# Kernel optimization log

Hardware: AMD Instinct MI355X
Metric: run time of the kernel (lower is better)

## Reference

```python
import jax, jax.numpy as jnp
import numpy as np

B, S, W = 128, 48, 12          # batch, sentences, words per sentence (= max_seq)
V, SYM, H = 32000, 128, 256    # vocab, symbol_size, hidden_size
E, R = 48, 24                  # entity_size, role_size
EPS = 1e-6


def _mlp(x, W1, b1, W2, b2):
    # repo MLP: tanh on both layers
    h = jnp.tanh(jnp.einsum('...e,eh->...h', x, W1) + b1)
    return jnp.tanh(jnp.einsum('...h,ho->...o', h, W2) + b2)


def _layer_norm(x, gain, bias):
    mu = x.mean(-1, keepdims=True)
    var = ((x - mu) ** 2).mean(-1, keepdims=True)
    return gain * (x - mu) / jnp.sqrt(var + EPS) + bias


def setup_inputs() -> dict:
    key = jax.random.key(0)
    ks = jax.random.split(key, 16)
    p = lambda k, shp: (jax.random.normal(k, shp) * 0.05).astype(jnp.float32)
    return {
        'story': jax.random.randint(ks[0], (B, S, W), 0, V),
        'query': jax.random.randint(ks[1], (B, W), 0, V),
        'word_embed': jax.random.uniform(ks[2], (V, SYM), minval=-0.1, maxval=0.1, dtype=jnp.float32),
        'pos_embed': jnp.ones((W, SYM), jnp.float32) / W,
        'Z': p(ks[3], (E, V)),
        # update-module MLPs: 2 entity heads, 3 role heads (stacked on dim 0)
        'ue_W1': p(ks[4], (2, SYM, H)), 'ue_b1': jnp.zeros((2, H), jnp.float32),
        'ue_W2': p(ks[5], (2, H, E)),   'ue_b2': jnp.zeros((2, E), jnp.float32),
        'ur_W1': p(ks[6], (3, SYM, H)), 'ur_b1': jnp.zeros((3, H), jnp.float32),
        'ur_W2': p(ks[7], (3, H, R)),   'ur_b2': jnp.zeros((3, R), jnp.float32),
        # inference-module MLPs
        'ie_W1': p(ks[8], (2, SYM, H)), 'ie_b1': jnp.zeros((2, H), jnp.float32),
        'ie_W2': p(ks[9], (2, H, E)),   'ie_b2': jnp.zeros((2, E), jnp.float32),
        'ir_W1': p(ks[10], (3, SYM, H)), 'ir_b1': jnp.zeros((3, H), jnp.float32),
        'ir_W2': p(ks[11], (3, H, R)),   'ir_b2': jnp.zeros((3, R), jnp.float32),
        # 3 optional LayerNorms over entity dim
        'ln_gain': jnp.ones((3, E), jnp.float32),
        'ln_bias': jnp.zeros((3, E), jnp.float32),
    }


def reference(story, query, word_embed, pos_embed, Z,
              ue_W1, ue_b1, ue_W2, ue_b2, ur_W1, ur_b1, ur_W2, ur_b2,
              ie_W1, ie_b1, ie_W2, ie_b2, ir_W1, ir_b1, ir_W2, ir_b2,
              ln_gain, ln_bias):
    # ---- UpdateModule ----
    sent = word_embed[story]                                   # [B,S,W,SYM]
    ssum = jnp.einsum('bswe,we->bse', sent, pos_embed)         # [B,S,SYM]
    e1 = _mlp(ssum, ue_W1[0], ue_b1[0], ue_W2[0], ue_b2[0])    # [B,S,E]
    e2 = _mlp(ssum, ue_W1[1], ue_b1[1], ue_W2[1], ue_b2[1])
    r1 = _mlp(ssum, ur_W1[0], ur_b1[0], ur_W2[0], ur_b2[0])    # [B,S,R]
    r2 = _mlp(ssum, ur_W1[1], ur_b1[1], ur_W2[1], ur_b2[1])
    r3 = _mlp(ssum, ur_W1[2], ur_b1[2], ur_W2[2], ur_b2[2])
    paW = jnp.einsum('bsr,bsf->bsrf', r1, e2)                  # partial_add_W
    paB = jnp.einsum('bsr,bsf->bsrf', r3, e1)                  # partial_add_B

    def step(TPR, x):
        e1i, e2i, r1i, r2i, r3i, paWi, paBi = x
        w_hat = jnp.einsum('be,br,berf->bf', e1i, r1i, TPR)
        m_hat = jnp.einsum('be,br,berf->bf', e1i, r2i, TPR)
        b_hat = jnp.einsum('be,br,berf->bf', e2i, r3i, TPR)
        write_op = paWi - jnp.einsum('br,bf->brf', r1i, w_hat)
        move_op = jnp.einsum('br,bf->brf', r2i, w_hat) - jnp.einsum('br,bf->brf', r2i, m_hat)
        backlink_op = paBi - jnp.einsum('br,bf->brf', r3i, b_hat)
        delta = (jnp.einsum('be,brf->berf', e1i, write_op + move_op)
                 + jnp.einsum('be,brf->berf', e2i, backlink_op))
        return TPR + delta, None

    xs = tuple(jnp.swapaxes(t, 0, 1) for t in (e1, e2, r1, r2, r3, paW, paB))  # step-major
    TPR0 = jnp.zeros((story.shape[0], E, R, E), jnp.float32)
    TPR, _ = jax.lax.scan(step, TPR0, xs)

    # ---- InferenceModule ----
    qsum = jnp.einsum('bwe,we->be', word_embed[query], pos_embed)  # [B,SYM]
    qe1 = _mlp(qsum, ie_W1[0], ie_b1[0], ie_W2[0], ie_b2[0])
    qr1 = _mlp(qsum, ir_W1[0], ir_b1[0], ir_W2[0], ir_b2[0])
    qr2 = _mlp(qsum, ir_W1[1], ir_b1[1], ir_W2[1], ir_b2[1])
    qr3 = _mlp(qsum, ir_W1[2], ir_b1[2], ir_W2[2], ir_b2[2])
    i1 = _layer_norm(jnp.einsum('be,br,berf->bf', qe1, qr1, TPR), ln_gain[0], ln_bias[0])
    i2 = _layer_norm(jnp.einsum('be,br,berf->bf', i1, qr2, TPR), ln_gain[1], ln_bias[1])
    i3 = _layer_norm(jnp.einsum('be,br,berf->bf', i2, qr3, TPR), ln_gain[2], ln_bias[2])
    logits = jnp.einsum('bf,fl->bl', i1 + i2 + i3, Z)              # [B,V]
    return logits
```

## Files before the change

### kernel.cpp

```cpp
#include <hip/hip_runtime.h>
#include <hip/hip_bf16.h>

#define B_ 128
#define S_ 48
#define W_ 12
#define V_ 32000
#define SYM_ 128
#define H_ 256
#define E_ 48
#define R_ 24
#define TM 32

typedef float f32x4 __attribute__((ext_vector_type(4)));

__device__ __forceinline__ float4 fma4(float s, float4 w, float4 a) {
    a.x = fmaf(s, w.x, a.x); a.y = fmaf(s, w.y, a.y);
    a.z = fmaf(s, w.z, a.z); a.w = fmaf(s, w.w, a.w);
    return a;
}

__device__ __forceinline__ void gl_lds16(const float* g, float* l) {
    __builtin_amdgcn_global_load_lds(
        (const __attribute__((address_space(1))) void*)g,
        (__attribute__((address_space(3))) void*)l, 16, 0, 0);
}

__device__ __forceinline__ float dot48(const float* A, const float* Bp) {
    const float4* a = reinterpret_cast<const float4*>(A);
    const float4* b4 = reinterpret_cast<const float4*>(Bp);
    float4 acc = {0.f, 0.f, 0.f, 0.f};
#pragma unroll
    for (int i = 0; i < 12; ++i) {
        float4 x = a[i], y = b4[i];
        acc.x = fmaf(x.x, y.x, acc.x); acc.y = fmaf(x.y, y.y, acc.y);
        acc.z = fmaf(x.z, y.z, acc.z); acc.w = fmaf(x.w, y.w, acc.w);
    }
    return (acc.x + acc.y) + (acc.z + acc.w);
}
__device__ __forceinline__ float dot24(const float* A, const float* Bp) {
    const float4* a = reinterpret_cast<const float4*>(A);
    const float4* b4 = reinterpret_cast<const float4*>(Bp);
    float4 acc = {0.f, 0.f, 0.f, 0.f};
#pragma unroll
    for (int i = 0; i < 6; ++i) {
        float4 x = a[i], y = b4[i];
        acc.x = fmaf(x.x, y.x, acc.x); acc.y = fmaf(x.y, y.y, acc.y);
        acc.z = fmaf(x.z, y.z, acc.z); acc.w = fmaf(x.w, y.w, acc.w);
    }
    return (acc.x + acc.y) + (acc.z + acc.w);
}

__global__ __launch_bounds__(128) void ssum_kernel(
    const int* __restrict__ story, const int* __restrict__ query,
    const float* __restrict__ we, const float* __restrict__ pe,
    float* __restrict__ ssum, float* __restrict__ qsum)
{
    int i = blockIdx.x;
    int c = threadIdx.x;
    const int* idxp;
    float* outp;
    if (i < B_ * S_) {
        idxp = story + (size_t)i * W_;
        outp = ssum + (size_t)i * SYM_;
    } else {
        int b = i - B_ * S_;
        idxp = query + (size_t)b * W_;
        outp = qsum + (size_t)b * SYM_;
    }
    float acc = 0.f;
#pragma unroll
    for (int w = 0; w < W_; ++w) {
        int id = idxp[w];
        acc = fmaf(we[(size_t)id * SYM_ + c], pe[w * SYM_ + c], acc);
    }
    outp[c] = acc;
}

template<int NQ>
__device__ __forceinline__ void mlp_layer2(
    int t, int row0, const float4* hs4, const float* __restrict__ W2,
    const float* __restrict__ b2, float* __restrict__ out)
{
    const float4* W2_4 = reinterpret_cast<const float4*>(W2);
    for (int idx = t; idx < TM * NQ; idx += 256) {
        int row = idx / NQ, q = idx - row * NQ;
        float4 cw0 = W2_4[0 * NQ + q];
        float4 cw1 = W2_4[1 * NQ + q];
        float4 cw2 = W2_4[2 * NQ + q];
        float4 cw3 = W2_4[3 * NQ + q];
        float4 a = {0, 0, 0, 0};
#pragma unroll 1
        for (int k4 = 0; k4 < H_ / 4 - 1; ++k4) {
            float4 nw0 = W2_4[(size_t)(4 * k4 + 4) * NQ + q];
            float4 nw1 = W2_4[(size_t)(4 * k4 + 5) * NQ + q];
            float4 nw2 = W2_4[(size_t)(4 * k4 + 6) * NQ + q];
            float4 nw3 = W2_4[(size_t)(4 * k4 + 7) * NQ + q];
            float4 h = hs4[row * 65 + k4];
            a = fma4(h.x, cw0, fma4(h.y, cw1, fma4(h.z, cw2, fma4(h.w, cw3, a))));
            cw0 = nw0; cw1 = nw1; cw2 = nw2; cw3 = nw3;
        }
        {
            float4 h = hs4[row * 65 + (H_ / 4 - 1)];
            a = fma4(h.x, cw0, fma4(h.y, cw1, fma4(h.z, cw2, fma4(h.w, cw3, a))));
        }
        float4 bv = reinterpret_cast<const float4*>(b2)[q];
        float4 o;
        o.x = tanhf(a.x + bv.x); o.y = tanhf(a.y + bv.y);
        o.z = tanhf(a.z + bv.z); o.w = tanhf(a.w + bv.w);
        reinterpret_cast<float4*>(out + (size_t)(row0 + row) * (NQ * 4))[q] = o;
    }
}

__global__ __launch_bounds__(256) void mlp_kernel(
    const float* __restrict__ x, int M,
    const float* __restrict__ W1e, const float* __restrict__ b1e,
    const float* __restrict__ W2e, const float* __restrict__ b2e,
    int nE,
    const float* __restrict__ W1r, const float* __restrict__ b1r,
    const float* __restrict__ W2r, const float* __restrict__ b2r,
    float* __restrict__ outE,
    float* __restrict__ outR)
{
    int m = blockIdx.y;
    int row0 = blockIdx.x * TM;
    const float *W1, *b1, *W2, *b2;
    float* out;
    int OUT;
    if (m < nE) {
        W1 = W1e + (size_t)m * SYM_ * H_;
        b1 = b1e + (size_t)m * H_;
        W2 = W2e + (size_t)m * H_ * E_;
        b2 = b2e + (size_t)m * E_;
        out = outE + (size_t)m * M * E_;
        OUT = E_;
    } else {
        int mr = m - nE;
        W1 = W1r + (size_t)mr * SYM_ * H_;
        b1 = b1r + (size_t)mr * H_;
        W2 = W2r + (size_t)mr * H_ * R_;
        b2 = b2r + (size_t)mr * R_;
        out = outR + (size_t)mr * M * R_;
        OUT = R_;
    }

    int t = threadIdx.x;
    const int wv = t >> 6;
    const int l = t & 63;

    __shared__ __align__(16) float4 pool4[TM * 65];
    float* wlds = reinterpret_cast<float*>(pool4);

    const int xoff = __builtin_amdgcn_readfirstlane((row0 + 8 * wv) * SYM_);
    const float* xw = x + xoff;

#define STAGE(c) { \
    const float* gsrc = W1 + (c) * 2048 + t * 4; \
    float* dst = wlds + ((c) % 3) * 2048 + wv * 256; \
    gl_lds16(gsrc, dst); \
    gl_lds16(gsrc + 1024, dst + 1024); }

#define CHUNK_COMPUTE(c_) { \
    const float* wl = wlds + ((c_) % 3) * 2048; \
    const float* xc = xw + (c_) * 8; \
    _Pragma("unroll") \
    for (int k = 0; k < 8; ++k) { \
        float4 w4 = *reinterpret_cast<const float4*>(wl + k * 256 + l * 4); \
        A0 = fma4(xc[0 * SYM_ + k], w4, A0); \
        A1 = fma4(xc[1 * SYM_ + k], w4, A1); \
        A2 = fma4(xc[2 * SYM_ + k], w4, A2); \
        A3 = fma4(xc[3 * SYM_ + k], w4, A3); \
        A4 = fma4(xc[4 * SYM_ + k], w4, A4); \
        A5 = fma4(xc[5 * SYM_ + k], w4, A5); \
        A6 = fma4(xc[6 * SYM_ + k], w4, A6); \
        A7 = fma4(xc[7 * SYM_ + k], w4, A7); \
    } }

    float4 A0 = {0, 0, 0, 0}, A1 = A0, A2 = A0, A3 = A0,
           A4 = A0, A5 = A0, A6 = A0, A7 = A0;

    STAGE(0)
    STAGE(1)

#pragma unroll 1
    for (int c = 0; c < 15; ++c) {
        asm volatile("s_waitcnt vmcnt(2)" ::: "memory");
        __builtin_amdgcn_s_barrier();
        if (c + 2 < 16) STAGE(c + 2)
        CHUNK_COMPUTE(c)
    }
    asm volatile("s_waitcnt vmcnt(0)" ::: "memory");
    __builtin_amdgcn_s_barrier();
    CHUNK_COMPUTE(15)
#undef CHUNK_COMPUTE
#undef STAGE

    __syncthreads();

    {
        float4 bb = reinterpret_cast<const float4*>(b1)[l];
        float4 v;
#define H1ROW(i, acc) \
        v.x = tanhf(acc.x + bb.x); v.y = tanhf(acc.y + bb.y); \
        v.z = tanhf(acc.z + bb.z); v.w = tanhf(acc.w + bb.w); \
        pool4[(8 * wv + i) * 65 + l] = v;
        H1ROW(0, A0) H1ROW(1, A1) H1ROW(2, A2) H1ROW(3, A3)
        H1ROW(4, A4) H1ROW(5, A5) H1ROW(6, A6) H1ROW(7, A7)
#undef H1ROW
    }
    __syncthreads();

    if (OUT == E_) mlp_layer2<12>(t, row0, pool4, W2, b2, out);
    else           mlp_layer2<6>(t, row0, pool4, W2, b2, out);
}

__global__ __launch_bounds__(256) void gram_kernel(
    const float* __restrict__ eg,
    const float* __restrict__ rg,
    const float* __restrict__ qe1,
    const float* __restrict__ qrr,
    float* __restrict__ Kg,
    float* __restrict__ qg)
{
    const int b = blockIdx.x;
    const int half = blockIdx.y;
    const int t = threadIdx.x;
    __shared__ __align__(16) float eL[2][48][52];
    __shared__ __align__(16) float rL[3][48][28];

    for (int i = t; i < 2 * 2304; i += 256) {
        int x = i / 2304, rem = i - x * 2304;
        eL[x][rem / 48][rem % 48] = eg[(size_t)x * B_ * 2304 + (size_t)b * 2304 + rem];
    }
    for (int i = t; i < 3 * 1152; i += 256) {
        int x = i / 1152, rem = i - x * 1152;
        rL[x][rem / 24][rem % 24] = rg[(size_t)x * B_ * 1152 + (size_t)b * 1152 + rem];
    }
    __syncthreads();

    for (int k = half * 564 + t; k < half * 564 + 564; k += 256) {
        int s2 = (int)((1.0f + sqrtf(1.0f + 8.0f * (float)k)) * 0.5f);
        while (s2 * (s2 - 1) / 2 > k) --s2;
        while ((s2 + 1) * s2 / 2 <= k) ++s2;
        int sp = k - s2 * (s2 - 1) / 2;

        float G11 = dot48(&eL[0][s2][0], &eL[0][sp][0]);
        float G12 = dot48(&eL[0][s2][0], &eL[1][sp][0]);
        float G21 = dot48(&eL[1][s2][0], &eL[0][sp][0]);
        float G22 = dot48(&eL[1][s2][0], &eL[1][sp][0]);
        float R11 = dot24(&rL[0][s2][0], &rL[0][sp][0]);
        float R12 = dot24(&rL[0][s2][0], &rL[1][sp][0]);
        float R13 = dot24(&rL[0][s2][0], &rL[2][sp][0]);
        float R21 = dot24(&rL[1][s2][0], &rL[0][sp][0]);
        float R22 = dot24(&rL[1][s2][0], &rL[1][sp][0]);
        float R23 = dot24(&rL[1][s2][0], &rL[2][sp][0]);
        float R31 = dot24(&rL[2][s2][0], &rL[0][sp][0]);
        float R32 = dot24(&rL[2][s2][0], &rL[1][sp][0]);
        float R33 = dot24(&rL[2][s2][0], &rL[2][sp][0]);

        float* kp = Kg + ((size_t)b * 1128 + k) * 12;
        float4 o0 = {G11 * R11, G11 * R12, G12 * R13, G11 * R21};
        float4 o1 = {G11 * R22, G12 * R23, G21 * R31, G21 * R32};
        float4 o2 = {G22 * R33, 0.f, 0.f, 0.f};
        *reinterpret_cast<float4*>(kp)     = o0;
        *reinterpret_cast<float4*>(kp + 4) = o1;
        *reinterpret_cast<float4*>(kp + 8) = o2;
    }

    if (half == 0) {
        float* dst = qg + (size_t)b * 544;
        for (int j = t; j < 528; j += 256) {
            if (j < 96) {
                int x = j / 48, sp = j % 48;
                const float* q = qe1 + b * 48;
                const float* v = &eL[x][sp][0];
                float a = 0.f;
#pragma unroll
                for (int kk = 0; kk < 48; ++kk) a = fmaf(q[kk], v[kk], a);
                dst[j] = a;
            } else {
                int jj = j - 96;
                int c = jj / 144;
                int rem = jj - c * 144;
                int rj = rem / 48, sp = rem % 48;
                const float* q = qrr + ((size_t)c * B_ + b) * 24;
                const float* v = &rL[rj][sp][0];
                float a = 0.f;
#pragma unroll
                for (int kk = 0; kk < 24; ++kk) a = fmaf(q[kk], v[kk], a);
                dst[j] = a;
            }
        }
    }
}

__global__ __launch_bounds__(512) void rec_kernel(
    const float* __restrict__ eg, const float* __restrict__ Kg,
    float* __restrict__ abcg)
{
    const int b = blockIdx.x;
    const int f0 = blockIdx.y * 24;
    const int t = threadIdx.x;
    __shared__ float acc[3][48][24];
    __shared__ float abc[3][48][24];
    __shared__ __align__(16) float KL[1128 * 12];

    for (int i = t; i < 1128 * 12; i += 512) KL[i] = Kg[(size_t)b * 1128 * 12 + i];
    for (int i = t; i < 3 * 48 * 24; i += 512) ((float*)acc)[i] = 0.f;
    const float* e1b = eg + (size_t)b * 2304;
    const float* e2b = eg + (size_t)B_ * 2304 + (size_t)b * 2304;
    __syncthreads();

    for (int s = 0; s < 48; ++s) {
        if (t < 24) {
            float w = acc[0][s][t], m = acc[1][s][t], bh = acc[2][s][t];
            abc[0][s][t] = e2b[s * 48 + f0 + t] - w;
            abc[1][s][t] = w - m;
            abc[2][s][t] = e1b[s * 48 + f0 + t] - bh;
        }
        __syncthreads();
        const int items = (47 - s) * 24;
        for (int idx = t; idx < items; idx += 512) {
            int d = idx / 24;
            int fl = idx - d * 24;
            int s2 = s + 1 + d;
            const float* kp = KL + (size_t)(s2 * (s2 - 1) / 2 + s) * 12;
            float4 k0 = *reinterpret_cast<const float4*>(kp);
            float4 k1 = *reinterpret_cast<const float4*>(kp + 4);
            float  k8 = kp[8];
            float av = abc[0][s][fl], bv = abc[1][s][fl], cv = abc[2][s][fl];
            acc[0][s2][fl] = fmaf(k0.x, av, fmaf(k0.y, bv, fmaf(k0.z, cv, acc[0][s2][fl])));
            acc[1][s2][fl] = fmaf(k0.w, av, fmaf(k1.x, bv, fmaf(k1.y, cv, acc[1][s2][fl])));
            acc[2][s2][fl] = fmaf(k1.z, av, fmaf(k1.w, bv, fmaf(k8,   cv, acc[2][s2][fl])));
        }
        __syncthreads();
    }
    for (int i = t; i < 3 * 48 * 24; i += 512) {
        int x = i / (48 * 24);
        int rem = i - x * 48 * 24;
        int s = rem / 24, fl = rem % 24;
        abcg[(size_t)b * 6912 + (size_t)x * 2304 + s * 48 + f0 + fl] = abc[x][s][fl];
    }
}

__global__ __launch_bounds__(256) void infer2_kernel(
    const float* __restrict__ abcg, const float* __restrict__ eg,
    const float* __restrict__ qgg,
    const float* __restrict__ ln_gain, const float* __restrict__ ln_bias,
    float* __restrict__ isum)
{
    const int b = blockIdx.x;
    const int t = threadIdx.x;
    __shared__ float abc[3][48][48];
    __shared__ __align__(16) float eL[2][48][52];
    __shared__ float qgL[544];
    __shared__ float alpha[3][48];
    __shared__ float gtmp[2][48];
    __shared__ float cur[48], xv[48], acc3[48];

    for (int i = t; i < 6912; i += 256) ((float*)abc)[i] = abcg[(size_t)b * 6912 + i];
    for (int i = t; i < 2 * 2304; i += 256) {
        int x = i / 2304, rem = i - x * 2304;
        eL[x][rem / 48][rem % 48] = eg[(size_t)x * B_ * 2304 + (size_t)b * 2304 + rem];
    }
    for (int i = t; i < 544; i += 256) qgL[i] = qgg[(size_t)b * 544 + i];
    if (t < 48) acc3[t] = 0.f;
    __syncthreads();

    for (int c = 0; c < 3; ++c) {
        if (c > 0) {
            for (int j = t; j < 96; j += 256) {
                int x = j / 48, sp = j % 48;
                const float* v = &eL[x][sp][0];
                float a = 0.f;
#pragma unroll
                for (int kk = 0; kk < 48; ++kk) a = fmaf(cur[kk], v[kk], a);
                gtmp[x][sp] = a;
            }
            __syncthreads();
        }
        if (t < 48) {
            float g1 = (c == 0) ? qgL[t] : gtmp[0][t];
            float g2 = (c == 0) ? qgL[48 + t] : gtmp[1][t];
            alpha[0][t] = g1 * qgL[96 + c * 144 + t];
            alpha[1][t] = g1 * qgL[96 + c * 144 + 48 + t];
            alpha[2][t] = g2 * qgL[96 + c * 144 + 96 + t];
        }
        __syncthreads();
        if (t < 48) {
            float p = 0.f;
            for (int sp = 0; sp < 48; ++sp) {
                p = fmaf(alpha[0][sp], abc[0][sp][t],
                    fmaf(alpha[1][sp], abc[1][sp][t],
                    fmaf(alpha[2][sp], abc[2][sp][t], p)));
            }
            xv[t] = p;
        }
        __syncthreads();
        if (t < 48) {
            float mu = 0.f;
#pragma unroll
            for (int jj = 0; jj < 48; ++jj) mu += xv[jj];
            mu *= (1.f / 48.f);
            float var = 0.f;
#pragma unroll
            for (int jj = 0; jj < 48; ++jj) { float d = xv[jj] - mu; var = fmaf(d, d, var); }
            var *= (1.f / 48.f);
            float inv = 1.f / sqrtf(var + 1e-6f);
            float o = ln_gain[c * 48 + t] * (xv[t] - mu) * inv + ln_bias[c * 48 + t];
            cur[t] = o;
            acc3[t] += o;
        }
        __syncthreads();
    }
    if (t < 48) isum[b * 48 + t] = acc3[t];
}

__global__ __launch_bounds__(256) void logits_kernel(
    const float* __restrict__ isum,
    const float* __restrict__ Z,
    float* __restrict__ out)
{
    int v = blockIdx.x * 256 + threadIdx.x;
    int b0 = blockIdx.y * (B_ / 4);
    float z[E_];
#pragma unroll
    for (int e = 0; e < E_; ++e) z[e] = Z[(size_t)e * V_ + v];
    for (int b = b0; b < b0 + B_ / 4; ++b) {
        float a = 0.f;
#pragma unroll
        for (int e = 0; e < E_; ++e) a = fmaf(isum[b * 48 + e], z[e], a);
        out[(size_t)b * V_ + v] = a;
    }
}

extern "C" void kernel_launch(void* const* d_in, const int* in_sizes, int n_in,
                              void* d_out, int out_size, void* d_ws, size_t ws_size,
                              hipStream_t stream) {
    const int* story  = (const int*)d_in[0];
    const int* query  = (const int*)d_in[1];
    const float* we   = (const float*)d_in[2];
    const float* pe   = (const float*)d_in[3];
    const float* Z    = (const float*)d_in[4];
    const float* ue_W1 = (const float*)d_in[5];
    const float* ue_b1 = (const float*)d_in[6];
    const float* ue_W2 = (const float*)d_in[7];
    const float* ue_b2 = (const float*)d_in[8];
    const float* ur_W1 = (const float*)d_in[9];
    const float* ur_b1 = (const float*)d_in[10];
    const float* ur_W2 = (const float*)d_in[11];
    const float* ur_b2 = (const float*)d_in[12];
    const float* ie_W1 = (const float*)d_in[13];
    const float* ie_b1 = (const float*)d_in[14];
    const float* ie_W2 = (const float*)d_in[15];
    const float* ie_b2 = (const float*)d_in[16];
    const float* ir_W1 = (const float*)d_in[17];
    const float* ir_b1 = (const float*)d_in[18];
    const float* ir_W2 = (const float*)d_in[19];
    const float* ir_b2 = (const float*)d_in[20];
    const float* ln_g  = (const float*)d_in[21];
    const float* ln_b  = (const float*)d_in[22];
    float* out = (float*)d_out;

    float* ws = (float*)d_ws;
    float* ssum = ws;
    float* qsum = ssum + (size_t)B_ * S_ * SYM_;
    float* eout = qsum + (size_t)B_ * SYM_;
    float* rout = eout + (size_t)2 * B_ * S_ * E_;
    float* qe1  = rout + (size_t)3 * B_ * S_ * R_;
    float* qrr  = qe1 + (size_t)B_ * E_;
    float* Kg   = qrr + (size_t)3 * B_ * R_;
    float* abcg = Kg + (size_t)B_ * 1128 * 12;
    float* qg   = abcg + (size_t)B_ * 6912;
    float* isum = qg + (size_t)B_ * 544;

    ssum_kernel<<<B_ * S_ + B_, 128, 0, stream>>>(story, query, we, pe, ssum, qsum);

    mlp_kernel<<<dim3((B_ * S_) / TM, 5), 256, 0, stream>>>(
        ssum, B_ * S_, ue_W1, ue_b1, ue_W2, ue_b2, 2,
        ur_W1, ur_b1, ur_W2, ur_b2, eout, rout);

    mlp_kernel<<<dim3(B_ / TM, 4), 256, 0, stream>>>(
        qsum, B_, ie_W1, ie_b1, ie_W2, ie_b2, 1,
        ir_W1, ir_b1, ir_W2, ir_b2, qe1, qrr);

    gram_kernel<<<dim3(B_, 2), 256, 0, stream>>>(eout, rout, qe1, qrr, Kg, qg);

    rec_kernel<<<dim3(B_, 2), 512, 0, stream>>>(eout, Kg, abcg);

    infer2_kernel<<<B_, 256, 0, stream>>>(abcg, eout, qg, ln_g, ln_b, isum);

    logits_kernel<<<dim3(V_ / 256, 4), 256, 0, stream>>>(isum, Z, out);
}
```

Measured before the change: 176.8 us.

## Stream MLP layer-1 weights into registers and double rows per block

The MLP first layer now loads W1 straight from global memory into registers with inline-asm dwordx4 loads in a two-stage double-buffered scheme, instead of staging through LDS with barriers. Each wave computes 16 rows instead of 8 (TM raised to 64), so each weight load is reused across more rows and half as many blocks are launched. The hidden-activation LDS buffer moves from padded rows to an XOR-swizzled layout to avoid bank conflicts. Risks include higher register pressure and lower occupancy from the 16 accumulators, fewer blocks to fill the GPU, and the need for the layout and grid sizing to stay consistent with TM.

```diff
diff --git a/kernel.cpp b/kernel.cpp
--- a/kernel.cpp
+++ b/kernel.cpp
@@ -9,7 +9,7 @@
 #define H_ 256
 #define E_ 48
 #define R_ 24
-#define TM 32
+#define TM 64
 
 typedef float f32x4 __attribute__((ext_vector_type(4)));
 
@@ -17,12 +17,6 @@
     a.x = fmaf(s, w.x, a.x); a.y = fmaf(s, w.y, a.y);
     a.z = fmaf(s, w.z, a.z); a.w = fmaf(s, w.w, a.w);
     return a;
-}
-
-__device__ __forceinline__ void gl_lds16(const float* g, float* l) {
-    __builtin_amdgcn_global_load_lds(
-        (const __attribute__((address_space(1))) void*)g,
-        (__attribute__((address_space(3))) void*)l, 16, 0, 0);
 }
 
 __device__ __forceinline__ float dot48(const float* A, const float* Bp) {
@@ -75,6 +69,31 @@
     }
     outp[c] = acc;
 }
+
+#define WLOAD4(R0,R1,R2,R3, PTR) \
+    asm volatile("global_load_dwordx4 %0, %4, off\n\t" \
+                 "global_load_dwordx4 %1, %4, off offset:1024\n\t" \
+                 "global_load_dwordx4 %2, %4, off offset:2048\n\t" \
+                 "global_load_dwordx4 %3, %4, off offset:3072" \
+                 : "=&v"(R0), "=&v"(R1), "=&v"(R2), "=&v"(R3) \
+                 : "v"(PTR))
+
+#define VWAIT4 { asm volatile("s_waitcnt vmcnt(4)" ::: "memory"); __builtin_amdgcn_sched_barrier(0); }
+#define VWAIT0 { asm volatile("s_waitcnt vmcnt(0)" ::: "memory"); __builtin_amdgcn_sched_barrier(0); }
+
+#define FMA1(AR, RIDX, KK, WREG) { \
+    float xs_ = xw[(RIDX) * SYM_ + (KK)]; \
+    f32x4 xb_ = {xs_, xs_, xs_, xs_}; \
+    AR = __builtin_elementwise_fma(xb_, WREG, AR); }
+
+#define FMAK(WREG, KK) \
+    FMA1(A0,0,KK,WREG)   FMA1(A1,1,KK,WREG)   FMA1(A2,2,KK,WREG)   FMA1(A3,3,KK,WREG) \
+    FMA1(A4,4,KK,WREG)   FMA1(A5,5,KK,WREG)   FMA1(A6,6,KK,WREG)   FMA1(A7,7,KK,WREG) \
+    FMA1(A8,8,KK,WREG)   FMA1(A9,9,KK,WREG)   FMA1(A10,10,KK,WREG) FMA1(A11,11,KK,WREG) \
+    FMA1(A12,12,KK,WREG) FMA1(A13,13,KK,WREG) FMA1(A14,14,KK,WREG) FMA1(A15,15,KK,WREG)
+
+#define FMAG(W0r,W1r,W2r,W3r, K0) { \
+    FMAK(W0r, (K0)+0) FMAK(W1r, (K0)+1) FMAK(W2r, (K0)+2) FMAK(W3r, (K0)+3) }
 
 template<int NQ>
 __device__ __forceinline__ void mlp_layer2(
@@ -95,12 +114,13 @@
             float4 nw1 = W2_4[(size_t)(4 * k4 + 5) * NQ + q];
             float4 nw2 = W2_4[(size_t)(4 * k4 + 6) * NQ + q];
             float4 nw3 = W2_4[(size_t)(4 * k4 + 7) * NQ + q];
-            float4 h = hs4[row * 65 + k4];
+            float4 h = hs4[row * 64 + (k4 ^ (row & 7))];
             a = fma4(h.x, cw0, fma4(h.y, cw1, fma4(h.z, cw2, fma4(h.w, cw3, a))));
             cw0 = nw0; cw1 = nw1; cw2 = nw2; cw3 = nw3;
         }
         {
-            float4 h = hs4[row * 65 + (H_ / 4 - 1)];
+            const int k4 = H_ / 4 - 1;
+            float4 h = hs4[row * 64 + (k4 ^ (row & 7))];
             a = fma4(h.x, cw0, fma4(h.y, cw1, fma4(h.z, cw2, fma4(h.w, cw3, a))));
         }
         float4 bv = reinterpret_cast<const float4*>(b2)[q];
@@ -143,74 +163,60 @@
         OUT = R_;
     }
 
-    int t = threadIdx.x;
+    const int t = threadIdx.x;
     const int wv = t >> 6;
     const int l = t & 63;
 
-    __shared__ __align__(16) float4 pool4[TM * 65];
-    float* wlds = reinterpret_cast<float*>(pool4);
-
-    const int xoff = __builtin_amdgcn_readfirstlane((row0 + 8 * wv) * SYM_);
+    __shared__ __align__(16) float4 hs4[64 * 64];
+
+    const int xoff = __builtin_amdgcn_readfirstlane((row0 + 16 * wv) * SYM_);
     const float* xw = x + xoff;
 
-#define STAGE(c) { \
-    const float* gsrc = W1 + (c) * 2048 + t * 4; \
-    float* dst = wlds + ((c) % 3) * 2048 + wv * 256; \
-    gl_lds16(gsrc, dst); \
-    gl_lds16(gsrc + 1024, dst + 1024); }
-
-#define CHUNK_COMPUTE(c_) { \
-    const float* wl = wlds + ((c_) % 3) * 2048; \
-    const float* xc = xw + (c_) * 8; \
-    _Pragma("unroll") \
-    for (int k = 0; k < 8; ++k) { \
-        float4 w4 = *reinterpret_cast<const float4*>(wl + k * 256 + l * 4); \
-        A0 = fma4(xc[0 * SYM_ + k], w4, A0); \
-        A1 = fma4(xc[1 * SYM_ + k], w4, A1); \
-        A2 = fma4(xc[2 * SYM_ + k], w4, A2); \
-        A3 = fma4(xc[3 * SYM_ + k], w4, A3); \
-        A4 = fma4(xc[4 * SYM_ + k], w4, A4); \
-        A5 = fma4(xc[5 * SYM_ + k], w4, A5); \
-        A6 = fma4(xc[6 * SYM_ + k], w4, A6); \
-        A7 = fma4(xc[7 * SYM_ + k], w4, A7); \
-    } }
-
-    float4 A0 = {0, 0, 0, 0}, A1 = A0, A2 = A0, A3 = A0,
-           A4 = A0, A5 = A0, A6 = A0, A7 = A0;
-
-    STAGE(0)
-    STAGE(1)
+    f32x4 A0 = {0.f, 0.f, 0.f, 0.f};
+    f32x4 A1 = A0, A2 = A0, A3 = A0, A4 = A0, A5 = A0, A6 = A0, A7 = A0,
+          A8 = A0, A9 = A0, A10 = A0, A11 = A0, A12 = A0, A13 = A0,
+          A14 = A0, A15 = A0;
+    f32x4 r0, r1, r2, r3, r4, r5, r6, r7;
+
+    const float* wq = W1 + 4 * l;
+    WLOAD4(r0, r1, r2, r3, wq);
+    WLOAD4(r4, r5, r6, r7, wq + 1024);
+    const float* wpA = wq + 2048;
+    const float* wpB = wq + 3072;
 
 #pragma unroll 1
-    for (int c = 0; c < 15; ++c) {
-        asm volatile("s_waitcnt vmcnt(2)" ::: "memory");
-        __builtin_amdgcn_s_barrier();
-        if (c + 2 < 16) STAGE(c + 2)
-        CHUNK_COMPUTE(c)
-    }
-    asm volatile("s_waitcnt vmcnt(0)" ::: "memory");
-    __builtin_amdgcn_s_barrier();
-    CHUNK_COMPUTE(15)
-#undef CHUNK_COMPUTE
-#undef STAGE
-
-    __syncthreads();
+    for (int i = 0; i < 15; ++i) {
+        const int k0 = 8 * i;
+        VWAIT4
+        FMAG(r0, r1, r2, r3, k0)
+        WLOAD4(r0, r1, r2, r3, wpA); wpA += 2048;
+        VWAIT4
+        FMAG(r4, r5, r6, r7, k0 + 4)
+        WLOAD4(r4, r5, r6, r7, wpB); wpB += 2048;
+    }
+    VWAIT4
+    FMAG(r0, r1, r2, r3, 120)
+    VWAIT0
+    FMAG(r4, r5, r6, r7, 124)
 
     {
         float4 bb = reinterpret_cast<const float4*>(b1)[l];
-        float4 v;
-#define H1ROW(i, acc) \
-        v.x = tanhf(acc.x + bb.x); v.y = tanhf(acc.y + bb.y); \
-        v.z = tanhf(acc.z + bb.z); v.w = tanhf(acc.w + bb.w); \
-        pool4[(8 * wv + i) * 65 + l] = v;
-        H1ROW(0, A0) H1ROW(1, A1) H1ROW(2, A2) H1ROW(3, A3)
-        H1ROW(4, A4) H1ROW(5, A5) H1ROW(6, A6) H1ROW(7, A7)
+#define H1ROW(RIDX, AR) { \
+        int row_ = 16 * wv + (RIDX); \
+        float4 v_; \
+        v_.x = tanhf(AR[0] + bb.x); v_.y = tanhf(AR[1] + bb.y); \
+        v_.z = tanhf(AR[2] + bb.z); v_.w = tanhf(AR[3] + bb.w); \
+        hs4[row_ * 64 + (l ^ (row_ & 7))] = v_; }
+        H1ROW(0, A0)   H1ROW(1, A1)   H1ROW(2, A2)   H1ROW(3, A3)
+        H1ROW(4, A4)   H1ROW(5, A5)   H1ROW(6, A6)   H1ROW(7, A7)
+        H1ROW(8, A8)   H1ROW(9, A9)   H1ROW(10, A10) H1ROW(11, A11)
+        H1ROW(12, A12) H1ROW(13, A13) H1ROW(14, A14) H1ROW(15, A15)
 #undef H1ROW
     }
     __syncthreads();
 
-    if (OUT == E_) mlp_layer2<12>(t, row0, pool4, W2, b2, out);
-    else           mlp_layer2<6>(t, row0, pool4, W2, b2, out);
+    if (OUT == E_) mlp_layer2<12>(t, row0, hs4, W2, b2, out);
+    else           mlp_layer2<6>(t, row0, hs4, W2, b2, out);
 }
 
 __global__ __launch_bounds__(256) void gram_kernel(
```

Result: slower. 200.7 us (+13.5%).

## Fuse gram and recurrence kernels, retile story MLP to six rows per wave

Applied to the files above, without the earlier changes.

Merges gram_kernel and rec_kernel into one 512-thread kernel. The pairwise K coefficients are now written straight to LDS instead of round-tripping through global memory, and e1/e2 are read from the already staged LDS copy. This removes a launch and the Kg global traffic, but each block now computes all 1128 pairs, so the work the two halves used to split is duplicated. The story MLP is templated to 6 rows per wave (24-row tiles), giving more blocks and fewer accumulators. Its FMAs now go through a vector elementwise fma builtin.

```diff
diff --git a/kernel.cpp b/kernel.cpp
--- a/kernel.cpp
+++ b/kernel.cpp
@@ -9,7 +9,6 @@
 #define H_ 256
 #define E_ 48
 #define R_ 24
-#define TM 32
 
 typedef float f32x4 __attribute__((ext_vector_type(4)));
 
@@ -17,6 +16,10 @@
     a.x = fmaf(s, w.x, a.x); a.y = fmaf(s, w.y, a.y);
     a.z = fmaf(s, w.z, a.z); a.w = fmaf(s, w.w, a.w);
     return a;
+}
+__device__ __forceinline__ f32x4 fmabc(float s, f32x4 w, f32x4 a) {
+    f32x4 sv = {s, s, s, s};
+    return __builtin_elementwise_fma(sv, w, a);
 }
 
 __device__ __forceinline__ void gl_lds16(const float* g, float* l) {
@@ -76,13 +79,13 @@
     outp[c] = acc;
 }
 
-template<int NQ>
+template<int NQ, int TMv>
 __device__ __forceinline__ void mlp_layer2(
     int t, int row0, const float4* hs4, const float* __restrict__ W2,
     const float* __restrict__ b2, float* __restrict__ out)
 {
     const float4* W2_4 = reinterpret_cast<const float4*>(W2);
-    for (int idx = t; idx < TM * NQ; idx += 256) {
+    for (int idx = t; idx < TMv * NQ; idx += 256) {
         int row = idx / NQ, q = idx - row * NQ;
         float4 cw0 = W2_4[0 * NQ + q];
         float4 cw1 = W2_4[1 * NQ + q];
@@ -111,6 +114,7 @@
     }
 }
 
+template<int ROWS>
 __global__ __launch_bounds__(256) void mlp_kernel(
     const float* __restrict__ x, int M,
     const float* __restrict__ W1e, const float* __restrict__ b1e,
@@ -121,8 +125,9 @@
     float* __restrict__ outE,
     float* __restrict__ outR)
 {
+    constexpr int TMv = ROWS * 4;
     int m = blockIdx.y;
-    int row0 = blockIdx.x * TM;
+    int row0 = blockIdx.x * TMv;
     const float *W1, *b1, *W2, *b2;
     float* out;
     int OUT;
@@ -143,14 +148,14 @@
         OUT = R_;
     }
 
-    int t = threadIdx.x;
+    const int t = threadIdx.x;
     const int wv = t >> 6;
     const int l = t & 63;
 
-    __shared__ __align__(16) float4 pool4[TM * 65];
+    __shared__ __align__(16) float4 pool4[TMv * 65];
     float* wlds = reinterpret_cast<float*>(pool4);
 
-    const int xoff = __builtin_amdgcn_readfirstlane((row0 + 8 * wv) * SYM_);
+    const int xoff = __builtin_amdgcn_readfirstlane((row0 + ROWS * wv) * SYM_);
     const float* xw = x + xoff;
 
 #define STAGE(c) { \
@@ -164,19 +169,21 @@
     const float* xc = xw + (c_) * 8; \
     _Pragma("unroll") \
     for (int k = 0; k < 8; ++k) { \
-        float4 w4 = *reinterpret_cast<const float4*>(wl + k * 256 + l * 4); \
-        A0 = fma4(xc[0 * SYM_ + k], w4, A0); \
-        A1 = fma4(xc[1 * SYM_ + k], w4, A1); \
-        A2 = fma4(xc[2 * SYM_ + k], w4, A2); \
-        A3 = fma4(xc[3 * SYM_ + k], w4, A3); \
-        A4 = fma4(xc[4 * SYM_ + k], w4, A4); \
-        A5 = fma4(xc[5 * SYM_ + k], w4, A5); \
-        A6 = fma4(xc[6 * SYM_ + k], w4, A6); \
-        A7 = fma4(xc[7 * SYM_ + k], w4, A7); \
+        f32x4 w4 = *reinterpret_cast<const f32x4*>(wl + k * 256 + l * 4); \
+        A0 = fmabc(xc[0 * SYM_ + k], w4, A0); \
+        A1 = fmabc(xc[1 * SYM_ + k], w4, A1); \
+        A2 = fmabc(xc[2 * SYM_ + k], w4, A2); \
+        A3 = fmabc(xc[3 * SYM_ + k], w4, A3); \
+        A4 = fmabc(xc[4 * SYM_ + k], w4, A4); \
+        A5 = fmabc(xc[5 * SYM_ + k], w4, A5); \
+        if constexpr (ROWS == 8) { \
+            A6 = fmabc(xc[6 * SYM_ + k], w4, A6); \
+            A7 = fmabc(xc[7 * SYM_ + k], w4, A7); \
+        } \
     } }
 
-    float4 A0 = {0, 0, 0, 0}, A1 = A0, A2 = A0, A3 = A0,
-           A4 = A0, A5 = A0, A6 = A0, A7 = A0;
+    f32x4 A0 = {0.f, 0.f, 0.f, 0.f};
+    f32x4 A1 = A0, A2 = A0, A3 = A0, A4 = A0, A5 = A0, A6 = A0, A7 = A0;
 
     STAGE(0)
     STAGE(1)
@@ -199,45 +206,54 @@
     {
         float4 bb = reinterpret_cast<const float4*>(b1)[l];
         float4 v;
-#define H1ROW(i, acc) \
-        v.x = tanhf(acc.x + bb.x); v.y = tanhf(acc.y + bb.y); \
-        v.z = tanhf(acc.z + bb.z); v.w = tanhf(acc.w + bb.w); \
-        pool4[(8 * wv + i) * 65 + l] = v;
-        H1ROW(0, A0) H1ROW(1, A1) H1ROW(2, A2) H1ROW(3, A3)
-        H1ROW(4, A4) H1ROW(5, A5) H1ROW(6, A6) H1ROW(7, A7)
+#define H1ROW(i, AR) \
+        v.x = tanhf(AR[0] + bb.x); v.y = tanhf(AR[1] + bb.y); \
+        v.z = tanhf(AR[2] + bb.z); v.w = tanhf(AR[3] + bb.w); \
+        pool4[(ROWS * wv + (i)) * 65 + l] = *reinterpret_cast<float4*>(&v);
+        H1ROW(0, A0) H1ROW(1, A1) H1ROW(2, A2)
+        H1ROW(3, A3) H1ROW(4, A4) H1ROW(5, A5)
+        if constexpr (ROWS == 8) {
+            H1ROW(6, A6) H1ROW(7, A7)
+        }
 #undef H1ROW
     }
     __syncthreads();
 
-    if (OUT == E_) mlp_layer2<12>(t, row0, pool4, W2, b2, out);
-    else           mlp_layer2<6>(t, row0, pool4, W2, b2, out);
-}
-
-__global__ __launch_bounds__(256) void gram_kernel(
+    if (OUT == E_) mlp_layer2<12, TMv>(t, row0, pool4, W2, b2, out);
+    else           mlp_layer2<6, TMv>(t, row0, pool4, W2, b2, out);
+}
+
+__global__ __launch_bounds__(512) void gramrec_kernel(
     const float* __restrict__ eg,
     const float* __restrict__ rg,
     const float* __restrict__ qe1,
     const float* __restrict__ qrr,
-    float* __restrict__ Kg,
-    float* __restrict__ qg)
+    float* __restrict__ qg,
+    float* __restrict__ abcg)
 {
     const int b = blockIdx.x;
     const int half = blockIdx.y;
+    const int f0 = half * 24;
     const int t = threadIdx.x;
+
     __shared__ __align__(16) float eL[2][48][52];
     __shared__ __align__(16) float rL[3][48][28];
-
-    for (int i = t; i < 2 * 2304; i += 256) {
+    __shared__ __align__(16) float KL[1128 * 12];
+    __shared__ float acc[3][48][24];
+    __shared__ float abc[3][48][24];
+
+    for (int i = t; i < 2 * 2304; i += 512) {
         int x = i / 2304, rem = i - x * 2304;
         eL[x][rem / 48][rem % 48] = eg[(size_t)x * B_ * 2304 + (size_t)b * 2304 + rem];
     }
-    for (int i = t; i < 3 * 1152; i += 256) {
+    for (int i = t; i < 3 * 1152; i += 512) {
         int x = i / 1152, rem = i - x * 1152;
         rL[x][rem / 24][rem % 24] = rg[(size_t)x * B_ * 1152 + (size_t)b * 1152 + rem];
     }
+    for (int i = t; i < 3 * 48 * 24; i += 512) ((float*)acc)[i] = 0.f;
     __syncthreads();
 
-    for (int k = half * 564 + t; k < half * 564 + 564; k += 256) {
+    for (int k = t; k < 1128; k += 512) {
         int s2 = (int)((1.0f + sqrtf(1.0f + 8.0f * (float)k)) * 0.5f);
         while (s2 * (s2 - 1) / 2 > k) --s2;
         while ((s2 + 1) * s2 / 2 <= k) ++s2;
@@ -257,18 +273,17 @@
         float R32 = dot24(&rL[2][s2][0], &rL[1][sp][0]);
         float R33 = dot24(&rL[2][s2][0], &rL[2][sp][0]);
 
-        float* kp = Kg + ((size_t)b * 1128 + k) * 12;
+        float* kp = KL + (size_t)k * 12;
         float4 o0 = {G11 * R11, G11 * R12, G12 * R13, G11 * R21};
         float4 o1 = {G11 * R22, G12 * R23, G21 * R31, G21 * R32};
-        float4 o2 = {G22 * R33, 0.f, 0.f, 0.f};
         *reinterpret_cast<float4*>(kp)     = o0;
         *reinterpret_cast<float4*>(kp + 4) = o1;
-        *reinterpret_cast<float4*>(kp + 8) = o2;
+        kp[8] = G22 * R33;
     }
 
     if (half == 0) {
         float* dst = qg + (size_t)b * 544;
-        for (int j = t; j < 528; j += 256) {
+        for (int j = t; j < 528; j += 512) {
             if (j < 96) {
                 int x = j / 48, sp = j % 48;
                 const float* q = qe1 + b * 48;
@@ -291,31 +306,14 @@
             }
         }
     }
-}
-
-__global__ __launch_bounds__(512) void rec_kernel(
-    const float* __restrict__ eg, const float* __restrict__ Kg,
-    float* __restrict__ abcg)
-{
-    const int b = blockIdx.x;
-    const int f0 = blockIdx.y * 24;
-    const int t = threadIdx.x;
-    __shared__ float acc[3][48][24];
-    __shared__ float abc[3][48][24];
-    __shared__ __align__(16) float KL[1128 * 12];
-
-    for (int i = t; i < 1128 * 12; i += 512) KL[i] = Kg[(size_t)b * 1128 * 12 + i];
-    for (int i = t; i < 3 * 48 * 24; i += 512) ((float*)acc)[i] = 0.f;
-    const float* e1b = eg + (size_t)b * 2304;
-    const float* e2b = eg + (size_t)B_ * 2304 + (size_t)b * 2304;
     __syncthreads();
 
     for (int s = 0; s < 48; ++s) {
         if (t < 24) {
             float w = acc[0][s][t], m = acc[1][s][t], bh = acc[2][s][t];
-            abc[0][s][t] = e2b[s * 48 + f0 + t] - w;
+            abc[0][s][t] = eL[1][s][f0 + t] - w;
             abc[1][s][t] = w - m;
-            abc[2][s][t] = e1b[s * 48 + f0 + t] - bh;
+            abc[2][s][t] = eL[0][s][f0 + t] - bh;
         }
         __syncthreads();
         const int items = (47 - s) * 24;
@@ -468,24 +466,21 @@
     float* rout = eout + (size_t)2 * B_ * S_ * E_;
     float* qe1  = rout + (size_t)3 * B_ * S_ * R_;
     float* qrr  = qe1 + (size_t)B_ * E_;
-    float* Kg   = qrr + (size_t)3 * B_ * R_;
-    float* abcg = Kg + (size_t)B_ * 1128 * 12;
+    float* abcg = qrr + (size_t)3 * B_ * R_;
     float* qg   = abcg + (size_t)B_ * 6912;
     float* isum = qg + (size_t)B_ * 544;
 
     ssum_kernel<<<B_ * S_ + B_, 128, 0, stream>>>(story, query, we, pe, ssum, qsum);
 
-    mlp_kernel<<<dim3((B_ * S_) / TM, 5), 256, 0, stream>>>(
+    mlp_kernel<6><<<dim3((B_ * S_) / 24, 5), 256, 0, stream>>>(
         ssum, B_ * S_, ue_W1, ue_b1, ue_W2, ue_b2, 2,
         ur_W1, ur_b1, ur_W2, ur_b2, eout, rout);
 
-    mlp_kernel<<<dim3(B_ / TM, 4), 256, 0, stream>>>(
+    mlp_kernel<8><<<dim3(B_ / 32, 4), 256, 0, stream>>>(
         qsum, B_, ie_W1, ie_b1, ie_W2, ie_b2, 1,
         ir_W1, ir_b1, ir_W2, ir_b2, qe1, qrr);
 
-    gram_kernel<<<dim3(B_, 2), 256, 0, stream>>>(eout, rout, qe1, qrr, Kg, qg);
-
-    rec_kernel<<<dim3(B_, 2), 512, 0, stream>>>(eout, Kg, abcg);
+    gramrec_kernel<<<dim3(B_, 2), 512, 0, stream>>>(eout, rout, qe1, qrr, qg, abcg);
 
     infer2_kernel<<<B_, 256, 0, stream>>>(abcg, eout, qg, ln_g, ln_b, isum);
 
```

New measurement: 170.4 us. 3.6% less time.
